# Kernel tuning notes

Measured on AMD Instinct MI355X. Metric: run time of the kernel, lower is better.

Reference implementation:

```python
import jax, jax.numpy as jnp
import numpy as np
import math

N, IFZ, NVZ, AHZ, QPZ, KZ, PEZ = 1024, 256, 64, 8, 4, 20, 20
NUM_FREQ = PEZ // 2
FREQ_INV = 50.0

def layer_norm(x, g, b, eps=1e-5):
    mu = x.mean(-1, keepdims=True)
    var = ((x - mu) ** 2).mean(-1, keepdims=True)
    return (x - mu) / jnp.sqrt(var + eps) * g + b

def setup_inputs() -> dict:
    key = jax.random.key(0)
    ks = jax.random.split(key, 8)
    x = jax.random.normal(ks[0], (N, IFZ), jnp.float32)
    affines = jax.random.normal(ks[1], (N, 3, 4), jnp.float32)
    prot_mask = jnp.ones((N,), dtype=bool)
    edge_index = jax.random.randint(ks[2], (N, KZ), 0, N, dtype=jnp.int32)
    s = 0.02
    w_nde = jax.random.normal(ks[3], (KZ * 3 * PEZ, NVZ), jnp.float32) * s
    b_nde = jnp.zeros((NVZ,), jnp.float32)
    w_q = jax.random.normal(ks[4], (IFZ + NVZ, AHZ * QPZ * 3), jnp.float32) * s
    w_v = jax.random.normal(ks[5], (IFZ + NVZ, AHZ * QPZ * IFZ), jnp.float32) * s
    ln_ag_g = jnp.ones((AHZ * QPZ * IFZ,), jnp.float32)
    ln_ag_b = jnp.zeros((AHZ * QPZ * IFZ,), jnp.float32)
    w_ag = jax.random.normal(ks[6], (AHZ * QPZ * IFZ, IFZ), jnp.float32) * s
    ln_en_g = jnp.ones((IFZ,), jnp.float32)
    ln_en_b = jnp.zeros((IFZ,), jnp.float32)
    return dict(x=x, affines=affines, prot_mask=prot_mask, edge_index=edge_index,
                w_nde=w_nde, b_nde=b_nde, w_q=w_q, w_v=w_v,
                ln_ag_g=ln_ag_g, ln_ag_b=ln_ag_b, w_ag=w_ag,
                ln_en_g=ln_en_g, ln_en_b=ln_en_b)

def reference(x, affines, prot_mask, edge_index, w_nde, b_nde, w_q, w_v,
              ln_ag_g, ln_ag_b, w_ag, ln_en_g, ln_en_b):
    dtype = x.dtype
    R = affines[:, :, :3]                                   # (N,3,3) rotation
    t = affines[:, :, 3]                                    # (N,3) translation
    positions = t
    # --- BackboneDistanceEmbedding (reconstructed): local neighbour vectors ---
    rel = positions[edge_index] - t[:, None, :]             # (N,K,3)
    local = jnp.einsum('nji,nkj->nki', R, rel)              # inverse-affine (R^T) (N,K,3)
    freqs = jnp.arange(1, NUM_FREQ + 1, dtype=dtype) / FREQ_INV
    ang = local[..., None] * freqs                          # (N,K,3,F)
    pe = jnp.concatenate([jnp.sin(ang), jnp.cos(ang)], -1)  # (N,K,3,PEZ)
    nv = jax.nn.relu(pe.reshape(x.shape[0], -1) @ w_nde + b_nde)  # (N,NVZ)
    nv = nv * prot_mask[:, None].astype(dtype)
    x_ne = jnp.concatenate([x, nv], axis=-1)                # (N,IFZ+NVZ)
    # --- query points in global frame ---
    q = (x_ne @ w_q).reshape(-1, 1, AHZ, QPZ, 3)
    q = jnp.einsum('nij,nkaqj->nkaqi', R, q) + t[:, None, None, None, :]
    gnp = positions[edge_index][:, :, None, None, :]        # (N,K,1,1,3)
    # --- L2-distance attention over neighbourhood ---
    scores = -jnp.linalg.norm(q - gnp, axis=-1).sum(-1)     # (N,K,AHZ)
    attn = jax.nn.softmax(scores, axis=1).astype(dtype)
    # --- value gather + weighted aggregation ---
    v = (x_ne @ w_v).reshape(-1, AHZ, QPZ, IFZ)
    v_ne = v[edge_index]                                    # (N,K,AHZ,QPZ,IFZ) -- big gather
    new = jnp.einsum('nkaqi,nka->naqi', v_ne, attn).reshape(x.shape[0], -1)
    new = layer_norm(new, ln_ag_g, ln_ag_b) @ w_ag          # dropout: eval mode => identity
    out = layer_norm(x + new / math.sqrt(2.0), ln_en_g, ln_en_b).astype(dtype)
    return out, edge_index
```

## Files before the change

kernel.cpp:

```cpp
#include <hip/hip_runtime.h>
#include <hip/hip_bf16.h>
#include <math.h>

#define NNODE 1024
#define IFZ   256
#define NVZ   64
#define AHZ   8
#define QPZ   4
#define KZ    20
#define PEZ   20
#define NF    10
#define XNE   320
#define VROW  8192
#define PEK   1216
#define SPLITS 8

typedef unsigned short ushort;
typedef __attribute__((ext_vector_type(8))) short    short8v;
typedef __attribute__((ext_vector_type(8))) ushort   ushort8v;
typedef __attribute__((ext_vector_type(4))) float    float4v;

static __device__ __forceinline__ ushort f2bf(float f) {
    unsigned u = __float_as_uint(f);
    unsigned r = 0x7FFFu + ((u >> 16) & 1u);
    return (ushort)((u + r) >> 16);
}
static __device__ __forceinline__ float bf2f(unsigned h) {
    return __uint_as_float(h << 16);
}

__global__ __launch_bounds__(256) void t_conv_g(
    const float* __restrict__ src, ushort* __restrict__ dst,
    int R, int C, int Rdst)
{
    __shared__ float t[32][33];
    const int c0 = blockIdx.x * 32, r0 = blockIdx.y * 32;
    const int tx = threadIdx.x, ty = threadIdx.y;
    #pragma unroll
    for (int i = 0; i < 4; ++i) {
        int r = r0 + ty + 8*i, c = c0 + tx;
        t[ty + 8*i][tx] = (r < R && c < C) ? src[(size_t)r * C + c] : 0.f;
    }
    __syncthreads();
    #pragma unroll
    for (int i = 0; i < 4; ++i)
        dst[(size_t)(c0 + ty + 8*i) * Rdst + r0 + tx] = f2bf(t[tx][ty + 8*i]);
}

__global__ __launch_bounds__(64) void k0_geom(
    const float* __restrict__ x, const float* __restrict__ aff,
    const int* __restrict__ edge,
    ushort* __restrict__ pe, ushort* __restrict__ xne_out,
    float* __restrict__ geom)
{
    const int n = blockIdx.x;
    const int lane = threadIdx.x;
    __shared__ float tn[KZ][3];
    __shared__ float r9[9], tt[3];

    if (lane < KZ) {
        int e = edge[n*KZ + lane];
        float a0 = aff[e*12 + 3], a1 = aff[e*12 + 7], a2 = aff[e*12 + 11];
        tn[lane][0] = a0; tn[lane][1] = a1; tn[lane][2] = a2;
        geom[n*72 + 12 + lane*3 + 0] = a0;
        geom[n*72 + 12 + lane*3 + 1] = a1;
        geom[n*72 + 12 + lane*3 + 2] = a2;
    } else if (lane < 29) {
        int q = lane - 20;
        float v = aff[n*12 + (q/3)*4 + (q%3)];
        r9[q] = v;
        geom[n*72 + q] = v;
    } else if (lane < 32) {
        float v = aff[n*12 + (lane-29)*4 + 3];
        tt[lane-29] = v;
        geom[n*72 + 9 + (lane-29)] = v;
    }
    {
        float4 xv = ((const float4*)(x + (size_t)n*IFZ))[lane];
        unsigned lo = f2bf(xv.x) | ((unsigned)f2bf(xv.y) << 16);
        unsigned hi = f2bf(xv.z) | ((unsigned)f2bf(xv.w) << 16);
        unsigned* p = (unsigned*)(xne_out + (size_t)n*XNE) + lane*2;
        p[0] = lo; p[1] = hi;
    }
    __syncthreads();

    if (lane < 60) {
        int k = lane / 3, i = lane % 3;
        float r0 = tn[k][0]-tt[0], r1 = tn[k][1]-tt[1], r2 = tn[k][2]-tt[2];
        float loc = r9[0+i]*r0 + r9[3+i]*r1 + r9[6+i]*r2;
        size_t base = (size_t)n*PEK + k*60 + i*20;
        #pragma unroll
        for (int p = 0; p < NF; p += 2) {
            float a0 = loc * (float)(p+1) * (1.0f/50.0f);
            float a1 = loc * (float)(p+2) * (1.0f/50.0f);
            unsigned us = f2bf(__sinf(a0)) | ((unsigned)f2bf(__sinf(a1)) << 16);
            unsigned uc = f2bf(__cosf(a0)) | ((unsigned)f2bf(__cosf(a1)) << 16);
            *(unsigned*)&pe[base + p]      = us;
            *(unsigned*)&pe[base + 10 + p] = uc;
        }
    }
    if (lane < 8)
        *(unsigned*)&pe[(size_t)n*PEK + 1200 + lane*2] = 0u;
}

#define EPI_BF16 0
#define EPI_F32S 1
#define EPI_RELU 2

template<int EPI>
__global__ __launch_bounds__(256) void gemm_bt(
    const ushort* __restrict__ A, const ushort* __restrict__ BT,
    ushort* __restrict__ Cb, float* __restrict__ Cf,
    const float* __restrict__ bias, int K, int ksplit, int ldc)
{
    __shared__ ushort As[64][40];
    __shared__ ushort Bs[64][40];
    const int bm = blockIdx.y * 64;
    const int bn = blockIdx.x * 64;
    const int tid = threadIdx.x;
    const int w = tid >> 6, lane = tid & 63;
    const int wr = w >> 1, wc = w & 1;
    const int lane15 = lane & 15, quad = lane >> 4;
    const int kbeg = blockIdx.z * ksplit;
    const int kend = kbeg + ksplit;

    const int sm = tid >> 2;
    const int sk = (tid & 3) * 8;

    float4v acc[2][2] = {};
    for (int k0 = kbeg; k0 < kend; k0 += 32) {
        *(ushort8v*)&As[sm][sk] = *(const ushort8v*)&A[(size_t)(bm + sm)*K + k0 + sk];
        *(ushort8v*)&Bs[sm][sk] = *(const ushort8v*)&BT[(size_t)(bn + sm)*K + k0 + sk];
        __syncthreads();
        short8v a0 = *(const short8v*)&As[wr*32      + lane15][quad*8];
        short8v a1 = *(const short8v*)&As[wr*32 + 16 + lane15][quad*8];
        short8v b0 = *(const short8v*)&Bs[wc*32      + lane15][quad*8];
        short8v b1 = *(const short8v*)&Bs[wc*32 + 16 + lane15][quad*8];
        acc[0][0] = __builtin_amdgcn_mfma_f32_16x16x32_bf16(a0, b0, acc[0][0], 0, 0, 0);
        acc[0][1] = __builtin_amdgcn_mfma_f32_16x16x32_bf16(a0, b1, acc[0][1], 0, 0, 0);
        acc[1][0] = __builtin_amdgcn_mfma_f32_16x16x32_bf16(a1, b0, acc[1][0], 0, 0, 0);
        acc[1][1] = __builtin_amdgcn_mfma_f32_16x16x32_bf16(a1, b1, acc[1][1], 0, 0, 0);
        __syncthreads();
    }

    const size_t splitoff = (EPI == EPI_F32S)
        ? (size_t)blockIdx.z * (size_t)NNODE * (size_t)ldc : 0;
    #pragma unroll
    for (int i = 0; i < 2; ++i) {
        #pragma unroll
        for (int j = 0; j < 2; ++j) {
            int col = bn + wc*32 + j*16 + lane15;
            #pragma unroll
            for (int r = 0; r < 4; ++r) {
                int row = bm + wr*32 + i*16 + quad*4 + r;
                float val = acc[i][j][r];
                if (EPI == EPI_RELU) val = fmaxf(val + bias[col], 0.f);
                if (EPI == EPI_F32S)
                    Cf[splitoff + (size_t)row*ldc + col] = val;
                else
                    Cb[(size_t)row*ldc + col] = f2bf(val);
            }
        }
    }
}

__global__ __launch_bounds__(256) void gemm_head(
    const ushort* __restrict__ Ab, const ushort* __restrict__ BTb,
    ushort* __restrict__ C)
{
    const int a = blockIdx.z;
    const ushort* A  = Ab  + (size_t)a * 1024 * XNE;
    const ushort* BT = BTb + (size_t)a * 1024 * XNE;
    __shared__ ushort As[64][40];
    __shared__ ushort Bs[64][40];
    const int bm = blockIdx.y * 64;
    const int bn = blockIdx.x * 64;
    const int tid = threadIdx.x;
    const int w = tid >> 6, lane = tid & 63;
    const int wr = w >> 1, wc = w & 1;
    const int lane15 = lane & 15, quad = lane >> 4;
    const int sm = tid >> 2;
    const int sk = (tid & 3) * 8;

    float4v acc[2][2] = {};
    for (int k0 = 0; k0 < XNE; k0 += 32) {
        *(ushort8v*)&As[sm][sk] = *(const ushort8v*)&A[(size_t)(bm + sm)*XNE + k0 + sk];
        *(ushort8v*)&Bs[sm][sk] = *(const ushort8v*)&BT[(size_t)(bn + sm)*XNE + k0 + sk];
        __syncthreads();
        short8v a0 = *(const short8v*)&As[wr*32      + lane15][quad*8];
        short8v a1 = *(const short8v*)&As[wr*32 + 16 + lane15][quad*8];
        short8v b0 = *(const short8v*)&Bs[wc*32      + lane15][quad*8];
        short8v b1 = *(const short8v*)&Bs[wc*32 + 16 + lane15][quad*8];
        acc[0][0] = __builtin_amdgcn_mfma_f32_16x16x32_bf16(a0, b0, acc[0][0], 0, 0, 0);
        acc[0][1] = __builtin_amdgcn_mfma_f32_16x16x32_bf16(a0, b1, acc[0][1], 0, 0, 0);
        acc[1][0] = __builtin_amdgcn_mfma_f32_16x16x32_bf16(a1, b0, acc[1][0], 0, 0, 0);
        acc[1][1] = __builtin_amdgcn_mfma_f32_16x16x32_bf16(a1, b1, acc[1][1], 0, 0, 0);
        __syncthreads();
    }

    #pragma unroll
    for (int i = 0; i < 2; ++i) {
        #pragma unroll
        for (int j = 0; j < 2; ++j) {
            int col = a*1024 + bn + wc*32 + j*16 + lane15;
            #pragma unroll
            for (int r = 0; r < 4; ++r) {
                int row = bm + wr*32 + i*16 + quad*4 + r;
                C[(size_t)row*VROW + col] = f2bf(acc[i][j][r]);
            }
        }
    }
}

__global__ __launch_bounds__(256) void k2_scores(
    const float* __restrict__ qbuf, const float* __restrict__ geom,
    float* __restrict__ attn_out)
{
    const int w = threadIdx.x >> 6, lane = threadIdx.x & 63;
    const int n = blockIdx.x * 4 + w;
    __shared__ float geo[4][72];
    __shared__ float qg[4][96];
    __shared__ float sc[4][160];

    if (lane < 72) geo[w][lane] = geom[n*72 + lane];
    __syncthreads();
    #pragma unroll
    for (int c = lane; c < 96; c += 64) {
        int i = c % 3, base = (c/3)*3;
        float q0 = qbuf[n*128 + base], q1 = qbuf[n*128 + base+1], q2 = qbuf[n*128 + base+2];
        qg[w][c] = geo[w][i*3+0]*q0 + geo[w][i*3+1]*q1 + geo[w][i*3+2]*q2 + geo[w][9+i];
    }
    __syncthreads();
    #pragma unroll
    for (int s = lane; s < 160; s += 64) {
        int k = s / 8, a = s % 8;
        float tx = geo[w][12+k*3+0], ty = geo[w][12+k*3+1], tz = geo[w][12+k*3+2];
        float acc = 0.f;
        #pragma unroll
        for (int qp = 0; qp < QPZ; ++qp) {
            int b = a*12 + qp*3;
            float dx = qg[w][b]   - tx;
            float dy = qg[w][b+1] - ty;
            float dz = qg[w][b+2] - tz;
            acc += sqrtf(dx*dx + dy*dy + dz*dz);
        }
        sc[w][a*20 + k] = -acc;
    }
    __syncthreads();
    if (lane < 8) {
        int a = lane;
        float m = -1e30f;
        #pragma unroll
        for (int k = 0; k < KZ; ++k) m = fmaxf(m, sc[w][a*20+k]);
        float e[KZ]; float sum = 0.f;
        #pragma unroll
        for (int k = 0; k < KZ; ++k) { e[k] = __expf(sc[w][a*20+k] - m); sum += e[k]; }
        float inv = 1.f / sum;
        #pragma unroll
        for (int k = 0; k < KZ; ++k) attn_out[n*160 + k*8 + a] = e[k]*inv;
    }
}

__global__ __launch_bounds__(256) void k_agg(
    const ushort* __restrict__ xne, const float* __restrict__ attn,
    const int* __restrict__ edge, ushort* __restrict__ agg)
{
    const int n = blockIdx.x;
    const int tid = threadIdx.x;
    __shared__ ushort xs[KZ][XNE];
    __shared__ float at[160];

    for (int s = tid; s < KZ*40; s += 256) {
        int k = s / 40, ch = s % 40;
        int e = edge[n*KZ + k];
        *(ushort8v*)&xs[k][ch*8] = *(const ushort8v*)&xne[(size_t)e*XNE + ch*8];
    }
    if (tid < 160) at[tid] = attn[n*160 + tid];
    __syncthreads();

    for (int s = tid; s < AHZ*40; s += 256) {
        int a = s / 40, ch = s % 40;
        float acc[8] = {};
        #pragma unroll 4
        for (int k = 0; k < KZ; ++k) {
            ushort8v p = *(const ushort8v*)&xs[k][ch*8];
            float wgt = at[k*8 + a];
            #pragma unroll
            for (int j = 0; j < 8; ++j)
                acc[j] += wgt * bf2f((ushort)p[j]);
        }
        ushort8v o;
        #pragma unroll
        for (int j = 0; j < 8; ++j) o[j] = (short)f2bf(acc[j]);
        *(ushort8v*)&agg[((size_t)a*NNODE + n)*XNE + ch*8] = o;
    }
}

__global__ __launch_bounds__(256) void k_ln(
    const ushort* __restrict__ nw, const float* __restrict__ g,
    const float* __restrict__ b, ushort* __restrict__ lnn)
{
    const int n = blockIdx.x;
    const int tid = threadIdx.x;
    __shared__ float wsum[4], wsq[4];
    __shared__ float s_mu, s_rstd;

    float vv[4][8];
    float lsum = 0.f, lsq = 0.f;
    #pragma unroll
    for (int ch = 0; ch < 4; ++ch) {
        int c = ch*2048 + tid*8;
        ushort8v p = *(const ushort8v*)(nw + (size_t)n*VROW + c);
        #pragma unroll
        for (int j = 0; j < 8; ++j) {
            float v = bf2f((ushort)p[j]);
            vv[ch][j] = v;
            lsum += v; lsq += v*v;
        }
    }
    #pragma unroll
    for (int off = 32; off > 0; off >>= 1) {
        lsum += __shfl_down(lsum, off, 64);
        lsq  += __shfl_down(lsq,  off, 64);
    }
    int wid = tid >> 6, lane = tid & 63;
    if (lane == 0) { wsum[wid] = lsum; wsq[wid] = lsq; }
    __syncthreads();
    if (tid == 0) {
        float ts = wsum[0]+wsum[1]+wsum[2]+wsum[3];
        float tq = wsq[0]+wsq[1]+wsq[2]+wsq[3];
        float mu = ts / (float)VROW;
        float var = tq / (float)VROW - mu*mu;
        s_mu = mu; s_rstd = rsqrtf(var + 1e-5f);
    }
    __syncthreads();
    float mu = s_mu, rstd = s_rstd;
    #pragma unroll
    for (int ch = 0; ch < 4; ++ch) {
        int c = ch*2048 + tid*8;
        ushort8v o;
        #pragma unroll
        for (int j = 0; j < 8; ++j)
            o[j] = (short)f2bf((vv[ch][j]-mu)*rstd*g[c+j] + b[c+j]);
        *(ushort8v*)&lnn[(size_t)n*VROW + c] = o;
    }
}

__global__ __launch_bounds__(256) void k6_final(
    const float* __restrict__ x, const float* __restrict__ tmp,
    const float* __restrict__ g, const float* __restrict__ b,
    const int* __restrict__ edge, float* __restrict__ out)
{
    const int n = blockIdx.x;
    const int tid = threadIdx.x;
    __shared__ float wsum[4], wsq[4];
    __shared__ float s_mu, s_rstd;
    float s = 0.f;
    #pragma unroll
    for (int sp = 0; sp < SPLITS; ++sp)
        s += tmp[sp*(NNODE*IFZ) + n*IFZ + tid];
    float val = x[n*IFZ + tid] + s * 0.70710678118654752f;
    float lsum = val, lsq = val*val;
    #pragma unroll
    for (int off = 32; off > 0; off >>= 1) {
        lsum += __shfl_down(lsum, off, 64);
        lsq  += __shfl_down(lsq,  off, 64);
    }
    int wid = tid >> 6, lane = tid & 63;
    if (lane == 0) { wsum[wid] = lsum; wsq[wid] = lsq; }
    __syncthreads();
    if (tid == 0) {
        float ts = wsum[0]+wsum[1]+wsum[2]+wsum[3];
        float tq = wsq[0]+wsq[1]+wsq[2]+wsq[3];
        float mu = ts / (float)IFZ;
        float var = tq / (float)IFZ - mu*mu;
        s_mu = mu; s_rstd = rsqrtf(var + 1e-5f);
    }
    __syncthreads();
    out[n*IFZ + tid] = (val - s_mu)*s_rstd*g[tid] + b[tid];
    if (tid < KZ)
        out[NNODE*IFZ + n*KZ + tid] = (float)edge[n*KZ + tid];
}

extern "C" void kernel_launch(void* const* d_in, const int* in_sizes, int n_in,
                              void* d_out, int out_size, void* d_ws, size_t ws_size,
                              hipStream_t stream)
{
    const float* x       = (const float*)d_in[0];
    const float* aff     = (const float*)d_in[1];
    const int*   edge    = (const int*)d_in[3];
    const float* w_nde   = (const float*)d_in[4];
    const float* b_nde   = (const float*)d_in[5];
    const float* w_q     = (const float*)d_in[6];
    const float* w_v     = (const float*)d_in[7];
    const float* ln_ag_g = (const float*)d_in[8];
    const float* ln_ag_b = (const float*)d_in[9];
    const float* w_ag    = (const float*)d_in[10];
    const float* ln_en_g = (const float*)d_in[11];
    const float* ln_en_b = (const float*)d_in[12];
    float* out = (float*)d_out;
    char*  w   = (char*)d_ws;

    ushort* xne_bf = (ushort*)(w + 0x0);
    float*  attn   = (float*) (w + 0xA0000);
    ushort* wvT    = (ushort*)(w + 0x140000);
    ushort* wagT   = (ushort*)(w + 0x640000);
    ushort* newbf  = (ushort*)(w + 0xA40000);
    ushort* lnn    = (ushort*)(w + 0x1A40000);
    float*  tmpk   = (float*) (w + 0x2A40000);
    ushort* pebf   = (ushort*)(w + 0x3240000);
    ushort* wndeT  = (ushort*)(w + 0x34A0000);
    ushort* wqT    = (ushort*)(w + 0x34C6000);
    float*  qbuf   = (float*) (w + 0x34DA000);
    float*  geom   = (float*) (w + 0x355A000);
    ushort* agg    = (ushort*)(w + 0x35A2000);

    hipLaunchKernelGGL(t_conv_g, dim3(VROW/32, XNE/32), dim3(32, 8), 0, stream,
                       w_v, wvT, XNE, VROW, XNE);
    hipLaunchKernelGGL(t_conv_g, dim3(IFZ/32, VROW/32), dim3(32, 8), 0, stream,
                       w_ag, wagT, VROW, IFZ, VROW);
    hipLaunchKernelGGL(t_conv_g, dim3(64/32, PEK/32), dim3(32, 8), 0, stream,
                       w_nde, wndeT, 1200, NVZ, PEK);
    hipLaunchKernelGGL(t_conv_g, dim3(128/32, XNE/32), dim3(32, 8), 0, stream,
                       w_q, wqT, XNE, 96, XNE);

    hipLaunchKernelGGL(k0_geom, dim3(NNODE), dim3(64), 0, stream,
                       x, aff, edge, pebf, xne_bf, geom);

    hipLaunchKernelGGL((gemm_bt<EPI_RELU>), dim3(1, NNODE/64, 1), dim3(256), 0, stream,
                       pebf, wndeT, xne_bf + IFZ, (float*)nullptr, b_nde,
                       PEK, PEK, XNE);

    hipLaunchKernelGGL((gemm_bt<EPI_F32S>), dim3(2, NNODE/64, 1), dim3(256), 0, stream,
                       xne_bf, wqT, (ushort*)nullptr, qbuf, (float*)nullptr,
                       XNE, XNE, 128);

    hipLaunchKernelGGL(k2_scores, dim3(NNODE/4), dim3(256), 0, stream,
                       qbuf, geom, attn);

    hipLaunchKernelGGL(k_agg, dim3(NNODE), dim3(256), 0, stream,
                       xne_bf, attn, edge, agg);

    hipLaunchKernelGGL(gemm_head, dim3(1024/64, NNODE/64, AHZ), dim3(256), 0, stream,
                       agg, wvT, newbf);

    hipLaunchKernelGGL(k_ln, dim3(NNODE), dim3(256), 0, stream,
                       newbf, ln_ag_g, ln_ag_b, lnn);

    hipLaunchKernelGGL((gemm_bt<EPI_F32S>), dim3(IFZ/64, NNODE/64, SPLITS), dim3(256), 0, stream,
                       lnn, wagT, (ushort*)nullptr, tmpk, (float*)nullptr,
                       VROW, VROW/SPLITS, IFZ);

    hipLaunchKernelGGL(k6_final, dim3(NNODE), dim3(256), 0, stream,
                       x, tmpk, ln_en_g, ln_en_b, edge, out);
}
```

Baseline: 189.6 us.

## Fold LayerNorm into output GEMM via row stats and precomputed weight vectors

Removes the standalone LayerNorm pass over the 1024x8192 head output. gemm_head now accumulates per-row sum and sum-of-squares with atomics, gamma is folded into the transposed w_ag, and a small gemv precomputes gamma·W and beta·W so the final kernel applies the mean/rstd correction algebraically. It also fuses score/softmax with aggregation and batches the four weight transposes into one launch. The cost is fp32 atomics, a one-pass variance formula that can lose precision, and rounding of the unnormalized output to bf16 before the GEMM.

New measurement: 236.4 us. +24.7%, slower.

```diff
diff --git a/kernel.cpp b/kernel.cpp
--- a/kernel.cpp
+++ b/kernel.cpp
@@ -29,34 +29,64 @@
     return __uint_as_float(h << 16);
 }
 
-__global__ __launch_bounds__(256) void t_conv_g(
-    const float* __restrict__ src, ushort* __restrict__ dst,
-    int R, int C, int Rdst)
-{
+struct TJob { const float* src; ushort* dst; const float* scl;
+              int R, C, gx, base, Rdst; };
+struct TJobs { TJob j[4]; };
+
+__global__ __launch_bounds__(256) void t_conv_all(TJobs P)
+{
+    const int bid = blockIdx.x;
+    int ji = 0;
+    #pragma unroll
+    for (int t = 1; t < 4; ++t) if (bid >= P.j[t].base) ji = t;
+    const TJob jb = P.j[ji];
+    const int rel = bid - jb.base;
+    const int bx = rel % jb.gx, by = rel / jb.gx;
+
     __shared__ float t[32][33];
-    const int c0 = blockIdx.x * 32, r0 = blockIdx.y * 32;
+    const int c0 = bx * 32, r0 = by * 32;
     const int tx = threadIdx.x, ty = threadIdx.y;
     #pragma unroll
     for (int i = 0; i < 4; ++i) {
         int r = r0 + ty + 8*i, c = c0 + tx;
-        t[ty + 8*i][tx] = (r < R && c < C) ? src[(size_t)r * C + c] : 0.f;
+        float v = (r < jb.R && c < jb.C) ? jb.src[(size_t)r * jb.C + c] : 0.f;
+        if (jb.scl && r < jb.R) v *= jb.scl[r];
+        t[ty + 8*i][tx] = v;
     }
     __syncthreads();
     #pragma unroll
     for (int i = 0; i < 4; ++i)
-        dst[(size_t)(c0 + ty + 8*i) * Rdst + r0 + tx] = f2bf(t[tx][ty + 8*i]);
+        jb.dst[(size_t)(c0 + ty + 8*i) * jb.Rdst + r0 + tx] = f2bf(t[tx][ty + 8*i]);
+}
+
+__global__ __launch_bounds__(256) void k_gemv(
+    const float* __restrict__ wag, const float* __restrict__ g,
+    const float* __restrict__ b, float* __restrict__ vpart)
+{
+    const int sp = blockIdx.x, j = threadIdx.x;
+    const float* base = wag + (size_t)sp * 256 * IFZ;
+    float vp = 0.f, bp = 0.f;
+    for (int r = 0; r < 256; ++r) {
+        float w = base[(size_t)r * IFZ + j];
+        vp += g[sp*256 + r] * w;
+        bp += b[sp*256 + r] * w;
+    }
+    vpart[(size_t)(sp*2 + 0) * IFZ + j] = vp;
+    vpart[(size_t)(sp*2 + 1) * IFZ + j] = bp;
 }
 
 __global__ __launch_bounds__(64) void k0_geom(
     const float* __restrict__ x, const float* __restrict__ aff,
     const int* __restrict__ edge,
     ushort* __restrict__ pe, ushort* __restrict__ xne_out,
-    float* __restrict__ geom)
+    float* __restrict__ geom, float* __restrict__ stats)
 {
     const int n = blockIdx.x;
     const int lane = threadIdx.x;
     __shared__ float tn[KZ][3];
     __shared__ float r9[9], tt[3];
+
+    if (n < 32) stats[n*64 + lane] = 0.f;
 
     if (lane < KZ) {
         int e = edge[n*KZ + lane];
@@ -166,7 +196,7 @@
 
 __global__ __launch_bounds__(256) void gemm_head(
     const ushort* __restrict__ Ab, const ushort* __restrict__ BTb,
-    ushort* __restrict__ C)
+    ushort* __restrict__ C, float* __restrict__ stats)
 {
     const int a = blockIdx.z;
     const ushort* A  = Ab  + (size_t)a * 1024 * XNE;
@@ -198,6 +228,36 @@
         __syncthreads();
     }
 
+    float rs[2][4], rq[2][4];
+    #pragma unroll
+    for (int i = 0; i < 2; ++i)
+        #pragma unroll
+        for (int r = 0; r < 4; ++r) {
+            float v0 = acc[i][0][r], v1 = acc[i][1][r];
+            rs[i][r] = v0 + v1;
+            rq[i][r] = v0*v0 + v1*v1;
+        }
+    #pragma unroll
+    for (int m = 1; m < 16; m <<= 1) {
+        #pragma unroll
+        for (int i = 0; i < 2; ++i)
+            #pragma unroll
+            for (int r = 0; r < 4; ++r) {
+                rs[i][r] += __shfl_xor(rs[i][r], m, 64);
+                rq[i][r] += __shfl_xor(rq[i][r], m, 64);
+            }
+    }
+    if (lane15 == 0) {
+        #pragma unroll
+        for (int i = 0; i < 2; ++i)
+            #pragma unroll
+            for (int r = 0; r < 4; ++r) {
+                int row = bm + wr*32 + i*16 + quad*4 + r;
+                atomicAdd(&stats[row*2    ], rs[i][r]);
+                atomicAdd(&stats[row*2 + 1], rq[i][r]);
+            }
+    }
+
     #pragma unroll
     for (int i = 0; i < 2; ++i) {
         #pragma unroll
@@ -212,70 +272,59 @@
     }
 }
 
-__global__ __launch_bounds__(256) void k2_scores(
+__global__ __launch_bounds__(256) void k_sc_agg(
     const float* __restrict__ qbuf, const float* __restrict__ geom,
-    float* __restrict__ attn_out)
-{
-    const int w = threadIdx.x >> 6, lane = threadIdx.x & 63;
-    const int n = blockIdx.x * 4 + w;
-    __shared__ float geo[4][72];
-    __shared__ float qg[4][96];
-    __shared__ float sc[4][160];
-
-    if (lane < 72) geo[w][lane] = geom[n*72 + lane];
-    __syncthreads();
-    #pragma unroll
-    for (int c = lane; c < 96; c += 64) {
-        int i = c % 3, base = (c/3)*3;
+    const ushort* __restrict__ xne, const int* __restrict__ edge,
+    ushort* __restrict__ agg)
+{
+    const int n = blockIdx.x;
+    const int tid = threadIdx.x;
+    __shared__ float geo[72], qg[96], sc[160], at[160];
+    __shared__ int es[KZ];
+    __shared__ ushort xs[KZ][XNE];
+
+    if (tid < 72) geo[tid] = geom[n*72 + tid];
+    else if (tid < 92) es[tid-72] = edge[n*KZ + (tid-72)];
+    __syncthreads();
+
+    if (tid < 96) {
+        int i = tid % 3, base = (tid/3)*3;
         float q0 = qbuf[n*128 + base], q1 = qbuf[n*128 + base+1], q2 = qbuf[n*128 + base+2];
-        qg[w][c] = geo[w][i*3+0]*q0 + geo[w][i*3+1]*q1 + geo[w][i*3+2]*q2 + geo[w][9+i];
-    }
-    __syncthreads();
-    #pragma unroll
-    for (int s = lane; s < 160; s += 64) {
-        int k = s / 8, a = s % 8;
-        float tx = geo[w][12+k*3+0], ty = geo[w][12+k*3+1], tz = geo[w][12+k*3+2];
+        qg[tid] = geo[i*3+0]*q0 + geo[i*3+1]*q1 + geo[i*3+2]*q2 + geo[9+i];
+    }
+    for (int s = tid; s < KZ*40; s += 256) {
+        int k = s / 40, ch = s % 40;
+        *(ushort8v*)&xs[k][ch*8] = *(const ushort8v*)&xne[(size_t)es[k]*XNE + ch*8];
+    }
+    __syncthreads();
+
+    if (tid < 160) {
+        int k = tid / 8, a = tid % 8;
+        float tx = geo[12+k*3+0], ty = geo[12+k*3+1], tz = geo[12+k*3+2];
         float acc = 0.f;
         #pragma unroll
         for (int qp = 0; qp < QPZ; ++qp) {
             int b = a*12 + qp*3;
-            float dx = qg[w][b]   - tx;
-            float dy = qg[w][b+1] - ty;
-            float dz = qg[w][b+2] - tz;
+            float dx = qg[b]   - tx;
+            float dy = qg[b+1] - ty;
+            float dz = qg[b+2] - tz;
             acc += sqrtf(dx*dx + dy*dy + dz*dz);
         }
-        sc[w][a*20 + k] = -acc;
-    }
-    __syncthreads();
-    if (lane < 8) {
-        int a = lane;
+        sc[a*20 + k] = -acc;
+    }
+    __syncthreads();
+    if (tid < 8) {
+        int a = tid;
         float m = -1e30f;
         #pragma unroll
-        for (int k = 0; k < KZ; ++k) m = fmaxf(m, sc[w][a*20+k]);
+        for (int k = 0; k < KZ; ++k) m = fmaxf(m, sc[a*20+k]);
         float e[KZ]; float sum = 0.f;
         #pragma unroll
-        for (int k = 0; k < KZ; ++k) { e[k] = __expf(sc[w][a*20+k] - m); sum += e[k]; }
+        for (int k = 0; k < KZ; ++k) { e[k] = __expf(sc[a*20+k] - m); sum += e[k]; }
         float inv = 1.f / sum;
         #pragma unroll
-        for (int k = 0; k < KZ; ++k) attn_out[n*160 + k*8 + a] = e[k]*inv;
-    }
-}
-
-__global__ __launch_bounds__(256) void k_agg(
-    const ushort* __restrict__ xne, const float* __restrict__ attn,
-    const int* __restrict__ edge, ushort* __restrict__ agg)
-{
-    const int n = blockIdx.x;
-    const int tid = threadIdx.x;
-    __shared__ ushort xs[KZ][XNE];
-    __shared__ float at[160];
-
-    for (int s = tid; s < KZ*40; s += 256) {
-        int k = s / 40, ch = s % 40;
-        int e = edge[n*KZ + k];
-        *(ushort8v*)&xs[k][ch*8] = *(const ushort8v*)&xne[(size_t)e*XNE + ch*8];
-    }
-    if (tid < 160) at[tid] = attn[n*160 + tid];
+        for (int k = 0; k < KZ; ++k) at[k*8 + a] = e[k]*inv;
+    }
     __syncthreads();
 
     for (int s = tid; s < AHZ*40; s += 256) {
@@ -296,60 +345,11 @@
     }
 }
 
-__global__ __launch_bounds__(256) void k_ln(
-    const ushort* __restrict__ nw, const float* __restrict__ g,
-    const float* __restrict__ b, ushort* __restrict__ lnn)
-{
-    const int n = blockIdx.x;
-    const int tid = threadIdx.x;
-    __shared__ float wsum[4], wsq[4];
-    __shared__ float s_mu, s_rstd;
-
-    float vv[4][8];
-    float lsum = 0.f, lsq = 0.f;
-    #pragma unroll
-    for (int ch = 0; ch < 4; ++ch) {
-        int c = ch*2048 + tid*8;
-        ushort8v p = *(const ushort8v*)(nw + (size_t)n*VROW + c);
-        #pragma unroll
-        for (int j = 0; j < 8; ++j) {
-            float v = bf2f((ushort)p[j]);
-            vv[ch][j] = v;
-            lsum += v; lsq += v*v;
-        }
-    }
-    #pragma unroll
-    for (int off = 32; off > 0; off >>= 1) {
-        lsum += __shfl_down(lsum, off, 64);
-        lsq  += __shfl_down(lsq,  off, 64);
-    }
-    int wid = tid >> 6, lane = tid & 63;
-    if (lane == 0) { wsum[wid] = lsum; wsq[wid] = lsq; }
-    __syncthreads();
-    if (tid == 0) {
-        float ts = wsum[0]+wsum[1]+wsum[2]+wsum[3];
-        float tq = wsq[0]+wsq[1]+wsq[2]+wsq[3];
-        float mu = ts / (float)VROW;
-        float var = tq / (float)VROW - mu*mu;
-        s_mu = mu; s_rstd = rsqrtf(var + 1e-5f);
-    }
-    __syncthreads();
-    float mu = s_mu, rstd = s_rstd;
-    #pragma unroll
-    for (int ch = 0; ch < 4; ++ch) {
-        int c = ch*2048 + tid*8;
-        ushort8v o;
-        #pragma unroll
-        for (int j = 0; j < 8; ++j)
-            o[j] = (short)f2bf((vv[ch][j]-mu)*rstd*g[c+j] + b[c+j]);
-        *(ushort8v*)&lnn[(size_t)n*VROW + c] = o;
-    }
-}
-
 __global__ __launch_bounds__(256) void k6_final(
     const float* __restrict__ x, const float* __restrict__ tmp,
     const float* __restrict__ g, const float* __restrict__ b,
-    const int* __restrict__ edge, float* __restrict__ out)
+    const int* __restrict__ edge, const float* __restrict__ stats,
+    const float* __restrict__ vpart, float* __restrict__ out)
 {
     const int n = blockIdx.x;
     const int tid = threadIdx.x;
@@ -359,7 +359,19 @@
     #pragma unroll
     for (int sp = 0; sp < SPLITS; ++sp)
         s += tmp[sp*(NNODE*IFZ) + n*IFZ + tid];
-    float val = x[n*IFZ + tid] + s * 0.70710678118654752f;
+    float vc = 0.f, bc = 0.f;
+    #pragma unroll 8
+    for (int sp = 0; sp < 32; ++sp) {
+        vc += vpart[(size_t)(sp*2 + 0)*IFZ + tid];
+        bc += vpart[(size_t)(sp*2 + 1)*IFZ + tid];
+    }
+    float S  = stats[n*2], S2 = stats[n*2 + 1];
+    float mu8 = S * (1.f/(float)VROW);
+    float var8 = S2 * (1.f/(float)VROW) - mu8*mu8;
+    float rstd8 = rsqrtf(var8 + 1e-5f);
+    float pre = rstd8*s - rstd8*mu8*vc + bc;
+
+    float val = x[n*IFZ + tid] + pre * 0.70710678118654752f;
     float lsum = val, lsq = val*val;
     #pragma unroll
     for (int off = 32; off > 0; off >>= 1) {
@@ -402,30 +414,31 @@
     char*  w   = (char*)d_ws;
 
     ushort* xne_bf = (ushort*)(w + 0x0);
-    float*  attn   = (float*) (w + 0xA0000);
+    float*  stats  = (float*) (w + 0xA0000);
+    float*  vpart  = (float*) (w + 0xA2000);
     ushort* wvT    = (ushort*)(w + 0x140000);
     ushort* wagT   = (ushort*)(w + 0x640000);
     ushort* newbf  = (ushort*)(w + 0xA40000);
-    ushort* lnn    = (ushort*)(w + 0x1A40000);
-    float*  tmpk   = (float*) (w + 0x2A40000);
-    ushort* pebf   = (ushort*)(w + 0x3240000);
-    ushort* wndeT  = (ushort*)(w + 0x34A0000);
-    ushort* wqT    = (ushort*)(w + 0x34C6000);
-    float*  qbuf   = (float*) (w + 0x34DA000);
-    float*  geom   = (float*) (w + 0x355A000);
-    ushort* agg    = (ushort*)(w + 0x35A2000);
-
-    hipLaunchKernelGGL(t_conv_g, dim3(VROW/32, XNE/32), dim3(32, 8), 0, stream,
-                       w_v, wvT, XNE, VROW, XNE);
-    hipLaunchKernelGGL(t_conv_g, dim3(IFZ/32, VROW/32), dim3(32, 8), 0, stream,
-                       w_ag, wagT, VROW, IFZ, VROW);
-    hipLaunchKernelGGL(t_conv_g, dim3(64/32, PEK/32), dim3(32, 8), 0, stream,
-                       w_nde, wndeT, 1200, NVZ, PEK);
-    hipLaunchKernelGGL(t_conv_g, dim3(128/32, XNE/32), dim3(32, 8), 0, stream,
-                       w_q, wqT, XNE, 96, XNE);
+    float*  tmpk   = (float*) (w + 0x1A40000);
+    ushort* pebf   = (ushort*)(w + 0x2240000);
+    ushort* wndeT  = (ushort*)(w + 0x24A0000);
+    ushort* wqT    = (ushort*)(w + 0x24C6000);
+    float*  qbuf   = (float*) (w + 0x24DA000);
+    float*  geom   = (float*) (w + 0x255A000);
+    ushort* agg    = (ushort*)(w + 0x25A2000);
+
+    TJobs P;
+    P.j[0] = { w_v,   wvT,   nullptr, XNE,  VROW, VROW/32, 0,    XNE  };
+    P.j[1] = { w_ag,  wagT,  ln_ag_g, VROW, IFZ,  IFZ/32,  2560, VROW };
+    P.j[2] = { w_nde, wndeT, nullptr, 1200, NVZ,  2,       4608, PEK  };
+    P.j[3] = { w_q,   wqT,   nullptr, XNE,  96,   4,       4684, XNE  };
+    hipLaunchKernelGGL(t_conv_all, dim3(4724), dim3(32, 8), 0, stream, P);
+
+    hipLaunchKernelGGL(k_gemv, dim3(32), dim3(256), 0, stream,
+                       w_ag, ln_ag_g, ln_ag_b, vpart);
 
     hipLaunchKernelGGL(k0_geom, dim3(NNODE), dim3(64), 0, stream,
-                       x, aff, edge, pebf, xne_bf, geom);
+                       x, aff, edge, pebf, xne_bf, geom, stats);
 
     hipLaunchKernelGGL((gemm_bt<EPI_RELU>), dim3(1, NNODE/64, 1), dim3(256), 0, stream,
                        pebf, wndeT, xne_bf + IFZ, (float*)nullptr, b_nde,
@@ -435,22 +448,16 @@
                        xne_bf, wqT, (ushort*)nullptr, qbuf, (float*)nullptr,
                        XNE, XNE, 128);
 
-    hipLaunchKernelGGL(k2_scores, dim3(NNODE/4), dim3(256), 0, stream,
-                       qbuf, geom, attn);
-
-    hipLaunchKernelGGL(k_agg, dim3(NNODE), dim3(256), 0, stream,
-                       xne_bf, attn, edge, agg);
+    hipLaunchKernelGGL(k_sc_agg, dim3(NNODE), dim3(256), 0, stream,
+                       qbuf, geom, xne_bf, edge, agg);
 
     hipLaunchKernelGGL(gemm_head, dim3(1024/64, NNODE/64, AHZ), dim3(256), 0, stream,
-                       agg, wvT, newbf);
-
-    hipLaunchKernelGGL(k_ln, dim3(NNODE), dim3(256), 0, stream,
-                       newbf, ln_ag_g, ln_ag_b, lnn);
+                       agg, wvT, newbf, stats);
 
     hipLaunchKernelGGL((gemm_bt<EPI_F32S>), dim3(IFZ/64, NNODE/64, SPLITS), dim3(256), 0, stream,
-                       lnn, wagT, (ushort*)nullptr, tmpk, (float*)nullptr,
+                       newbf, wagT, (ushort*)nullptr, tmpk, (float*)nullptr,
                        VROW, VROW/SPLITS, IFZ);
 
     hipLaunchKernelGGL(k6_final, dim3(NNODE), dim3(256), 0, stream,
-                       x, tmpk, ln_en_g, ln_en_b, edge, out);
-}
+                       x, tmpk, ln_en_g, ln_en_b, edge, stats, vpart, out);
+}
```
